# Performance work log

Measured on AMD Instinct MI355X. Metric: run time of the kernel, lower is better.

## Reference

```python
import jax, jax.numpy as jnp
import numpy as np
import math

B, U, IN, H = 4096, 6, 256, 600
IKS, IVS, NIH = 64, 400, 1           # input attention key/value sizes, heads
CKS, CQS, NCH = 32, 32, 4            # comm attention key/query sizes, heads
CVS = H                              # comm value size forced to hidden_size
K = 4                                # top-k active units


@jax.custom_vjp
def blocked_grad(x, mask):
    return x

def _bg_fwd(x, mask):
    return x, mask

def _bg_bwd(mask, g):
    return (g * mask, jnp.zeros_like(mask))

blocked_grad.defvjp(_bg_fwd, _bg_bwd)


def _gll(x, w):
    # GroupLinearLayer: per-unit bmm, x (B,U,din) @ w (U,din,dout) -> (B,U,dout)
    return jnp.einsum('bud,udo->buo', x, w)


def setup_inputs() -> dict:
    key = jax.random.key(0)
    ks = jax.random.split(key, 16)
    r = lambda i, shape: (0.02 * jax.random.normal(ks[i], shape)).astype(jnp.float32)
    return dict(
        x=jax.random.normal(ks[0], (B, 1, IN), jnp.float32),
        hs=jax.random.normal(ks[1], (B, U, H), jnp.float32),
        Wk=r(2, (IN, NIH * IKS)), bk=jnp.zeros((NIH * IKS,), jnp.float32),
        Wv=r(3, (IN, NIH * IVS)), bv=jnp.zeros((NIH * IVS,), jnp.float32),
        Wq=r(4, (U, H, NIH * IKS)),
        x2h_w=r(5, (U, IVS, 3 * H)), h2h_w=r(6, (U, H, 3 * H)),
        Wq_=r(7, (U, H, NCH * CQS)), Wk_=r(8, (U, H, NCH * CKS)),
        Wv_=r(9, (U, H, NCH * CVS)), Wout=r(10, (U, NCH * CVS, CVS)),
    )


def reference(x, hs, Wk, bk, Wv, bv, Wq, x2h_w, h2h_w, Wq_, Wk_, Wv_, Wout):
    h_old = hs
    # append null input along dim 1 -> (B,2,IN)
    xcat = jnp.concatenate([x, jnp.zeros_like(x)], axis=1)
    # ---- input attention + top-k mask ----
    key_l = (xcat @ Wk + bk).reshape(B, 2, NIH, IKS).transpose(0, 2, 1, 3)   # (B,1,2,ks)
    val_l = (xcat @ Wv + bv).reshape(B, 2, NIH, IVS).mean(axis=2)             # (B,2,vs) mean over heads
    qry_l = _gll(hs, Wq).reshape(B, U, NIH, IKS).transpose(0, 2, 1, 3)        # (B,1,U,ks)
    scores = jnp.einsum('bhuk,bhnk->bhun', qry_l, key_l) / math.sqrt(IKS)
    scores = scores.mean(axis=1)                                               # (B,U,2)
    not_null = scores[:, :, 0]
    _, idx = jax.lax.top_k(not_null, K)                                        # (B,K)
    mask = jnp.zeros((B, U), jnp.float32).at[jnp.arange(B)[:, None], idx].set(1.0)
    probs = jax.nn.softmax(scores, axis=-1)                                    # dropout is identity (eval)
    inputs = jnp.einsum('bun,bnv->buv', probs, val_l) * mask[:, :, None]       # (B,U,vs)
    # ---- GroupGRU cell ----
    gx = _gll(inputs, x2h_w)
    gh = _gll(hs, h2h_w)
    i_r, i_i, i_n = jnp.split(gx, 3, axis=2)
    h_r, h_i, h_n = jnp.split(gh, 3, axis=2)
    rg = jax.nn.sigmoid(i_r + h_r)
    ig = jax.nn.sigmoid(i_i + h_i)
    ng = jnp.tanh(i_n + rg * h_n)
    hs = ng + ig * (hs - ng)
    # ---- communication attention (with blocked_grad) ----
    h_b = blocked_grad(hs, mask[:, :, None])
    q = _gll(h_b, Wq_).reshape(B, U, NCH, CQS).transpose(0, 2, 1, 3)   # (B,4,U,32)
    k = _gll(h_b, Wk_).reshape(B, U, NCH, CKS).transpose(0, 2, 1, 3)
    v = _gll(h_b, Wv_).reshape(B, U, NCH, CVS).transpose(0, 2, 1, 3)   # (B,4,U,600)
    att = jax.nn.softmax(jnp.einsum('bhuk,bhnk->bhun', q, k) / math.sqrt(CKS), axis=-1)
    att = att * mask[:, None, :, None]   # zero rows of inactive query units
    ctx = jnp.einsum('bhun,bhnv->bhuv', att, v).transpose(0, 2, 1, 3).reshape(B, U, NCH * CVS)
    ctx = _gll(ctx, Wout) + h_b
    m = mask[:, :, None]
    return m * ctx + (1.0 - m) * h_old
```

## Files before the change

kernel.cpp:

```cpp
#include <hip/hip_runtime.h>
#include <math.h>

typedef unsigned short u16;
typedef __attribute__((ext_vector_type(8))) short short8;
typedef __attribute__((ext_vector_type(4))) float f32x4;

constexpr int NB   = 4096;
constexpr int NU   = 6;
constexpr int NIN  = 256;
constexpr int NH   = 600;
constexpr int IKS  = 64;
constexpr int IVS  = 400;
constexpr int NCH  = 4;
constexpr int CVS  = 600;
constexpr int KTOP = 4;

constexpr int KVW  = IKS + IVS;
constexpr int QKW  = 256;
constexpr int VW   = NCH * CVS;

constexpr int KGRU = 1024;
constexpr int HOFS = 416;
constexpr int NGATE = 640;
constexpr int KH   = 640;
constexpr int VN   = 2432;
constexpr int BC   = 2048;
constexpr int NCHUNK = NB / BC;

constexpr long OFF_KV   = 0;
constexpr long OFF_QRY  = OFF_KV   + (long)NB * KVW;
constexpr long OFF_C0   = OFF_QRY  + (long)NB * NU * IKS;
constexpr long OFF_C1   = OFF_C0   + (long)NB * NU;
constexpr long OFF_MASK = OFF_C1   + (long)NB * NU;
constexpr long OFF_QK   = OFF_MASK + (long)NB * NU;
constexpr long OFF_ATTW = OFF_QK   + (long)NB * NU * QKW;
constexpr long OFF_HNBF = OFF_ATTW + (long)NB * NCH * NU * NU;
constexpr long OFF_WQK  = OFF_HNBF + (long)NU * NB * KH / 2;
constexpr long OFF_WV   = OFF_WQK  + (long)NU * QKW * KH / 2;
constexpr long OFF_WOUT = OFF_WV   + (long)NU * VN * KH / 2;
constexpr long OFF_WGRU = OFF_WOUT + (long)NU * NGATE * VN / 2;
constexpr long OFF_AGRU = OFF_WGRU + (long)NU * 3 * NGATE * KGRU / 2;
constexpr long OFF_VBUF = OFF_WGRU;

__device__ __forceinline__ u16 f2bf(float f) {
    unsigned int x = __float_as_uint(f);
    x += 0x7FFFu + ((x >> 16) & 1u);
    return (u16)(x >> 16);
}
__device__ __forceinline__ float bf2f(u16 u) {
    return __uint_as_float(((unsigned int)u) << 16);
}
__device__ __forceinline__ void gl_lds16(const u16* g, u16* l) {
    __builtin_amdgcn_global_load_lds(
        (const __attribute__((address_space(1))) void*)g,
        (__attribute__((address_space(3))) void*)l, 16, 0, 0);
}
__device__ __forceinline__ void xcd_swz(int& bx, int& by, int& bz)
{
    const int gx = gridDim.x, gy = gridDim.y, gz = gridDim.z;
    const int n = gx * gy * gz;
    if (n & 7) return;
    int lid = bx + gx * (by + gy * bz);
    const int q = n >> 3;
    int w = (lid & 7) * q + (lid >> 3);
    bx = w % gx; int rest = w / gx;
    by = rest % gy; bz = rest / gy;
}

#define WAITVM_(N) asm volatile("s_waitcnt vmcnt(" #N ")" ::: "memory")
#define WAITVM(N)  WAITVM_(N)
#define WAITLG()   asm volatile("s_waitcnt lgkmcnt(0)" ::: "memory")
#define SBAR()     do { __builtin_amdgcn_sched_barrier(0); \
                        __builtin_amdgcn_s_barrier();      \
                        __builtin_amdgcn_sched_barrier(0); } while (0)

__global__ __launch_bounds__(256)
void wtrans_kernel(const float* __restrict__ src, long s_u, int s_ld, int s_colofs,
                   int Ksrc, int Nsub,
                   u16* __restrict__ dst, long d_u, int d_ld, int d_nofs, int d_kofs,
                   int gdiv, int s_gcol, int d_gnofs)
{
    __shared__ float tile[32][33];
    int z = blockIdx.z;
    int u = z, g = 0;
    if (gdiv > 1) { u = z / gdiv; g = z % gdiv; }
    const int k0 = blockIdx.x * 32, n0 = blockIdx.y * 32;
    const int t  = threadIdx.x;
    const int scol = s_colofs + g * s_gcol;
    const int dnof = d_nofs + g * d_gnofs;
    const float* S = src + (long)u * s_u;
    u16* D = dst + (long)u * d_u;
    #pragma unroll
    for (int r = 0; r < 4; r++) {
        int kk = r * 8 + (t >> 5), nn = t & 31;
        float v = 0.f;
        if (k0 + kk < Ksrc && n0 + nn < Nsub)
            v = S[(long)(k0 + kk) * s_ld + scol + n0 + nn];
        tile[kk][nn] = v;
    }
    __syncthreads();
    #pragma unroll
    for (int r = 0; r < 4; r++) {
        int nn = r * 8 + (t >> 5), kk = t & 31;
        if (n0 + nn < Nsub)
            D[(long)(dnof + n0 + nn) * d_ld + d_kofs + k0 + kk] = f2bf(tile[kk][nn]);
    }
}

__global__ __launch_bounds__(256)
void gemm_kv_kernel(const float* __restrict__ x,
                    const float* __restrict__ Wk, const float* __restrict__ bk,
                    const float* __restrict__ Wv, const float* __restrict__ bv,
                    float* __restrict__ kvout)
{
    const int m0 = blockIdx.x * 64;
    const int n0 = blockIdx.y * 64;
    const int tid = threadIdx.x;
    const int tm = tid / 16, tn = tid % 16;
    constexpr int K = NIN, N = KVW;

    __shared__ __align__(16) float As[32][72];
    __shared__ __align__(16) float Ws[32][68];
    float acc[4][4] = {};

    for (int k0 = 0; k0 < K; k0 += 32) {
        #pragma unroll
        for (int s2 = 0; s2 < 2; s2++) {
            int s = tid * 2 + s2;
            int row = s >> 3, kc = s & 7;
            float4 v = *(const float4*)&x[(long)(m0 + row) * K + k0 + kc * 4];
            As[kc*4+0][row] = v.x; As[kc*4+1][row] = v.y;
            As[kc*4+2][row] = v.z; As[kc*4+3][row] = v.w;
        }
        #pragma unroll
        for (int s2 = 0; s2 < 2; s2++) {
            int s = tid * 2 + s2;
            int kr = s >> 4, c4 = s & 15;
            int cg = n0 + c4 * 4;
            float4 v = {0,0,0,0};
            if (cg < IKS)    v = *(const float4*)&Wk[(long)(k0+kr)*IKS + cg];
            else if (cg < N) v = *(const float4*)&Wv[(long)(k0+kr)*IVS + (cg - IKS)];
            *(float4*)&Ws[kr][c4*4] = v;
        }
        __syncthreads();
        #pragma unroll
        for (int kk = 0; kk < 32; kk++) {
            float4 a4 = *(const float4*)&As[kk][tm*4];
            float4 w4 = *(const float4*)&Ws[kk][tn*4];
            float av[4] = {a4.x,a4.y,a4.z,a4.w}, wv[4] = {w4.x,w4.y,w4.z,w4.w};
            #pragma unroll
            for (int i = 0; i < 4; i++)
                #pragma unroll
                for (int j = 0; j < 4; j++)
                    acc[i][j] = fmaf(av[i], wv[j], acc[i][j]);
        }
        __syncthreads();
    }
    #pragma unroll
    for (int i = 0; i < 4; i++) {
        int row = m0 + tm*4 + i;
        #pragma unroll
        for (int j = 0; j < 4; j++) {
            int cg = n0 + tn*4 + j;
            if (cg < N) {
                float bias = (cg < IKS) ? bk[cg] : bv[cg - IKS];
                kvout[(long)row*N + cg] = acc[i][j] + bias;
            }
        }
    }
}

__global__ __launch_bounds__(256)
void gemm_qry_kernel(const float* __restrict__ A,
                     const float* __restrict__ W,
                     float* __restrict__ C)
{
    const int u  = blockIdx.z;
    const int m0 = blockIdx.x * 64;
    const int tid = threadIdx.x;
    const int tm = tid / 16, tn = tid % 16;
    constexpr int K = NH, N = IKS;
    const long lda = (long)NU * NH;

    __shared__ __align__(16) float As[32][72];
    __shared__ __align__(16) float Ws[32][68];
    const float* Au = A + (long)u * K;
    const float* Wu = W + (long)u * K * N;
    float acc[4][4] = {};

    for (int k0 = 0; k0 < K; k0 += 32) {
        #pragma unroll
        for (int s2 = 0; s2 < 2; s2++) {
            int s = tid * 2 + s2;
            int row = s >> 3, kc = s & 7;
            float4 v = {0,0,0,0};
            if (k0 + kc*4 < K)
                v = *(const float4*)&Au[(long)(m0 + row) * lda + k0 + kc * 4];
            As[kc*4+0][row] = v.x; As[kc*4+1][row] = v.y;
            As[kc*4+2][row] = v.z; As[kc*4+3][row] = v.w;
        }
        #pragma unroll
        for (int s2 = 0; s2 < 2; s2++) {
            int s = tid * 2 + s2;
            int kr = s >> 4, c4 = s & 15;
            float4 v = {0,0,0,0};
            if (k0 + kr < K)
                v = *(const float4*)&Wu[(long)(k0 + kr) * N + c4 * 4];
            *(float4*)&Ws[kr][c4*4] = v;
        }
        __syncthreads();
        #pragma unroll
        for (int kk = 0; kk < 32; kk++) {
            float4 a4 = *(const float4*)&As[kk][tm*4];
            float4 w4 = *(const float4*)&Ws[kk][tn*4];
            float av[4] = {a4.x,a4.y,a4.z,a4.w}, wv[4] = {w4.x,w4.y,w4.z,w4.w};
            #pragma unroll
            for (int i = 0; i < 4; i++)
                #pragma unroll
                for (int j = 0; j < 4; j++)
                    acc[i][j] = fmaf(av[i], wv[j], acc[i][j]);
        }
        __syncthreads();
    }
    #pragma unroll
    for (int i = 0; i < 4; i++) {
        int row = m0 + tm*4 + i;
        #pragma unroll
        for (int j = 0; j < 4; j++) {
            int c = tn*4 + j;
            C[(long)row*(NU*IKS) + (long)u*IKS + c] = acc[i][j];
        }
    }
}

__global__ __launch_bounds__(64)
void score_kernel(const float* __restrict__ qry, const float* __restrict__ kv,
                  const float* __restrict__ bk,
                  float* __restrict__ c0, float* __restrict__ c1,
                  float* __restrict__ maskf)
{
    const int b = blockIdx.x;
    const int t = threadIdx.x;
    __shared__ float s0s[NU], s1s[NU];

    float k0v = kv[(long)b*KVW + t];
    float bkv = bk[t];
    for (int u = 0; u < NU; u++) {
        float q  = qry[((long)b*NU + u)*IKS + t];
        float p0 = q * k0v, p1 = q * bkv;
        #pragma unroll
        for (int off = 32; off > 0; off >>= 1) {
            p0 += __shfl_down(p0, off);
            p1 += __shfl_down(p1, off);
        }
        if (t == 0) { s0s[u] = p0 * 0.125f; s1s[u] = p1 * 0.125f; }
    }
    __syncthreads();
    if (t < NU) {
        int u = t;
        float su = s0s[u];
        int rank = 0;
        #pragma unroll
        for (int j = 0; j < NU; j++) {
            float sj = s0s[j];
            if (sj > su || (sj == su && j < u)) rank++;
        }
        float m = (rank < KTOP) ? 1.0f : 0.0f;
        float a = s0s[u], bb = s1s[u];
        float mx = fmaxf(a, bb);
        float e0 = expf(a - mx), e1 = expf(bb - mx);
        float p0 = e0 / (e0 + e1);
        c0[(long)b*NU + u]    = m * p0;
        c1[(long)b*NU + u]    = m * (1.0f - p0);
        maskf[(long)b*NU + u] = m;
    }
}

__global__ __launch_bounds__(256)
void prep_gruA_kernel(const float* __restrict__ kv, const float* __restrict__ bv,
                      const float* __restrict__ hs,
                      const float* __restrict__ c0, const float* __restrict__ c1,
                      u16* __restrict__ Ag)
{
    long id = (long)blockIdx.x * 256 + threadIdx.x;
    const long total = (long)NU * NB * (KGRU / 8);
    if (id >= total) return;
    int k8 = (int)(id % (KGRU / 8));
    int b  = (int)((id / (KGRU / 8)) % NB);
    int u  = (int)(id / ((long)(KGRU / 8) * NB));
    int k  = k8 * 8;
    u16 o[8];
    if (k < IVS) {
        float cv0 = c0[(long)b*NU + u], cv1 = c1[(long)b*NU + u];
        const float* kp = kv + (long)b*KVW + IKS + k;
        const float* bp = bv + k;
        #pragma unroll
        for (int i = 0; i < 8; i++) o[i] = f2bf(cv0*kp[i] + cv1*bp[i]);
    } else if (k >= HOFS && k < HOFS + NH) {
        const float* hp = hs + ((long)b*NU + u)*NH + (k - HOFS);
        #pragma unroll
        for (int i = 0; i < 8; i++) o[i] = f2bf(hp[i]);
    } else {
        #pragma unroll
        for (int i = 0; i < 8; i++) o[i] = 0;
    }
    *(short8*)&Ag[id * 8] = *(const short8*)o;
}

__global__ __launch_bounds__(256, 3)
void gru_mfma_kernel(const u16* __restrict__ Ag, const u16* __restrict__ Wg,
                     const float* __restrict__ hs, u16* __restrict__ hnbf)
{
    int bx = blockIdx.x, by = blockIdx.y, bz = blockIdx.z;
    xcd_swz(bx, by, bz);
    const int u  = bz;
    const int m0 = bx * 128;
    const int n0 = by * 32;
    const int tid = threadIdx.x;
    const int wid = tid >> 6, lane = tid & 63;
    const int wm = wid >> 1, wn = wid & 1;
    const int lrow = lane & 15, lkq = lane >> 4;
    const int srow = lane >> 2;
    const int scs  = (((lane & 3) ^ ((lane >> 3) & 3)) * 8);
    const int cofs = ((lkq ^ ((lrow >> 1) & 3)) * 8);

    __shared__ __align__(16) u16 As[3][128 * 32];
    __shared__ __align__(16) u16 Bs[3][128 * 32];

    const u16* Au = Ag + (long)u * NB * KGRU;
    const u16* Wu = Wg + (long)u * 3 * NGATE * KGRU;

    f32x4 aR[4], aI[4], aNX[4], aNH[4];
    #pragma unroll
    for (int m = 0; m < 4; m++) {
        aR[m] = (f32x4){0,0,0,0}; aI[m] = (f32x4){0,0,0,0};
        aNX[m] = (f32x4){0,0,0,0}; aNH[m] = (f32x4){0,0,0,0};
    }

#define GSTAGE(BUF, T) do {                                                   \
        const long kk0 = (long)(T) * 32;                                      \
        _Pragma("unroll")                                                     \
        for (int i2 = 0; i2 < 2; i2++) {                                      \
            int R = wid*32 + i2*16;                                           \
            int row = R + srow;                                               \
            gl_lds16(Au + (long)(m0 + row)*KGRU + kk0 + scs,                  \
                     &As[BUF][R * 32]);                                       \
            int g = row >> 5; if (g > 2) g = 2;     \
            int rn = row & 31;                                                \
            gl_lds16(Wu + ((long)g*NGATE + n0 + rn)*KGRU + kk0 + scs,         \
                     &Bs[BUF][R * 32]);                                       \
        }                                                                     \
    } while (0)

#define GCOMPUTE(BUF, T) do {                                                 \
        __builtin_amdgcn_s_setprio(1);                                        \
        short8 af[4], bR, bI, bN;                                             \
        _Pragma("unroll")                                                     \
        for (int m = 0; m < 4; m++)                                           \
            af[m] = *(const short8*)&As[BUF][(wm*64 + m*16 + lrow)*32 + cofs];\
        {                                                                     \
            int nr = wn*16 + lrow;                                            \
            bR = *(const short8*)&Bs[BUF][(0*32 + nr)*32 + cofs];             \
            bI = *(const short8*)&Bs[BUF][(1*32 + nr)*32 + cofs];             \
            bN = *(const short8*)&Bs[BUF][(2*32 + nr)*32 + cofs];             \
        }                                                                     \
        _Pragma("unroll")                                                     \
        for (int m = 0; m < 4; m++) {                                         \
            aR[m] = __builtin_amdgcn_mfma_f32_16x16x32_bf16(af[m], bR, aR[m], 0, 0, 0); \
            aI[m] = __builtin_amdgcn_mfma_f32_16x16x32_bf16(af[m], bI, aI[m], 0, 0, 0); \
        }                                                                     \
        if ((T) < HOFS/32) {                                                  \
            _Pragma("unroll")                                                 \
            for (int m = 0; m < 4; m++)                                       \
                aNX[m] = __builtin_amdgcn_mfma_f32_16x16x32_bf16(af[m], bN, aNX[m], 0, 0, 0); \
        } else {                                                              \
            _Pragma("unroll")                                                 \
            for (int m = 0; m < 4; m++)                                       \
                aNH[m] = __builtin_amdgcn_mfma_f32_16x16x32_bf16(af[m], bN, aNH[m], 0, 0, 0); \
        }                                                                     \
        __builtin_amdgcn_s_setprio(0);                                        \
    } while (0)

    constexpr int KSTEPS = KGRU / 32;
    GSTAGE(0, 0);
    int bc = 0, bn = 1;
    for (int t = 0; t < KSTEPS - 1; ++t) {
        GSTAGE(bn, t + 1);
        WAITVM(4); SBAR();
        GCOMPUTE(bc, t);
        bc = bn; bn = (bn == 2) ? 0 : bn + 1;
    }
    WAITVM(0); SBAR();
    GCOMPUTE(bc, KSTEPS - 1);
#undef GCOMPUTE
#undef GSTAGE

    #pragma unroll
    for (int m = 0; m < 4; m++) {
        #pragma unroll
        for (int r = 0; r < 4; r++) {
            int row = m0 + wm*64 + m*16 + lkq*4 + r;
            int col = n0 + wn*16 + lrow;
            u16 ov = 0;
            if (col < NH) {
                float rg = 1.0f / (1.0f + expf(-aR[m][r]));
                float ig = 1.0f / (1.0f + expf(-aI[m][r]));
                float ng = tanhf(aNX[m][r] + rg * aNH[m][r]);
                float h  = hs[((long)row*NU + u)*NH + col];
                ov = f2bf(ng + ig * (h - ng));
            }
            hnbf[(long)u*NB*KH + (long)row*KH + col] = ov;
        }
    }
}

template<int EPI>
__global__ __launch_bounds__(256, 2)
void mfgemm_kernel(const u16* __restrict__ A, long sAu, int lda,
                   const u16* __restrict__ Bw, long sBu, int ldb,
                   float* __restrict__ Cf, u16* __restrict__ C16,
                   long sCu, int ldc, int ksteps,
                   const float* __restrict__ maskf,
                   const u16* __restrict__ hnbf,
                   const float* __restrict__ hs,
                   int bbase)
{
    int bx = blockIdx.x, by = blockIdx.y, bz = blockIdx.z;
    xcd_swz(bx, by, bz);
    const int u  = bz;
    const int m0 = bx * 128;
    const int n0 = by * 128;
    const int tid = threadIdx.x;
    const int wid = tid >> 6, lane = tid & 63;
    const int wm = wid >> 1, wn = wid & 1;
    const int lrow = lane & 15, lkq = lane >> 4;
    const int l8 = lane & 7, lr8 = lane >> 3;
    const int rsw = lrow & 7;

    __shared__ __align__(16) u16 As[2][128 * 64];
    __shared__ __align__(16) u16 Bs[2][128 * 64];

    const u16* Au = A + (long)u * sAu;
    const u16* Bu = Bw + (long)u * sBu;

    f32x4 acc[4][4];
    #pragma unroll
    for (int m = 0; m < 4; m++)
        #pragma unroll
        for (int n = 0; n < 4; n++) acc[m][n] = (f32x4){0,0,0,0};

#define MSTAGE(BUF, KS) do {                                                  \
        const long kk0 = (long)(KS) * 64;                                     \
        _Pragma("unroll")                                                     \
        for (int i2 = 0; i2 < 4; i2++) {                                      \
            int rw = i2*32 + wid*8 + lr8;                                     \
            int co = ((l8 ^ (rw & 7)) * 8);                                   \
            gl_lds16(Au + (long)(m0 + rw)*lda + kk0 + co,                     \
                     &As[BUF][(i2*32 + wid*8) * 64]);                         \
            gl_lds16(Bu + (long)(n0 + rw)*ldb + kk0 + co,                     \
                     &Bs[BUF][(i2*32 + wid*8) * 64]);                         \
        }                                                                     \
    } while (0)

#define MCOMPUTE(BUF) do {                                                    \
        __builtin_amdgcn_s_setprio(1);                                        \
        _Pragma("unroll")                                                     \
        for (int ks2 = 0; ks2 < 2; ks2++) {                                   \
            const int cofs = (((ks2*4 + lkq) ^ rsw) * 8);                     \
            short8 af[4], bfr[4];                                             \
            _Pragma("unroll")                                                 \
            for (int m = 0; m < 4; m++)                                       \
                af[m] = *(const short8*)&As[BUF][(wm*64 + m*16 + lrow)*64 + cofs]; \
            _Pragma("unroll")                                                 \
            for (int n = 0; n < 4; n++)                                       \
                bfr[n] = *(const short8*)&Bs[BUF][(wn*64 + n*16 + lrow)*64 + cofs]; \
            _Pragma("unroll")                                                 \
            for (int m = 0; m < 4; m++)                                       \
                _Pragma("unroll")                                             \
                for (int n = 0; n < 4; n++)                                   \
                    acc[m][n] = __builtin_amdgcn_mfma_f32_16x16x32_bf16(af[m], bfr[n], acc[m][n], 0, 0, 0); \
        }                                                                     \
        __builtin_amdgcn_s_setprio(0);                                        \
    } while (0)

#define MPH(BUF, T, W) do {                                                   \
        if ((T) + 1 < ksteps) MSTAGE((BUF)^1, (T)+1);                         \
        WAITVM(W); SBAR();                                                    \
        MCOMPUTE(BUF);                                                        \
        WAITLG(); SBAR();                                                     \
    } while (0)

    MSTAGE(0, 0);
    int t = 0;
    for (; t + 2 < ksteps; t += 2) { MPH(0, t, 8); MPH(1, t+1, 8); }
    if (t + 2 == ksteps) { MPH(0, t, 8); MPH(1, t+1, 0); }
    else                 { MPH(0, t, 0); }
#undef MPH
#undef MCOMPUTE
#undef MSTAGE

    #pragma unroll
    for (int m = 0; m < 4; m++) {
        #pragma unroll
        for (int r = 0; r < 4; r++) {
            int row = m0 + wm*64 + m*16 + lkq*4 + r;
            #pragma unroll
            for (int n = 0; n < 4; n++) {
                int col = n0 + wn*64 + n*16 + lrow;
                float v = acc[m][n][r];
                if (EPI == 0) {
                    Cf[(long)u*sCu + (long)row*ldc + col] = v;
                } else if (EPI == 2) {
                    C16[(long)u*sCu + (long)row*ldc + col] = f2bf(v);
                } else {
                    if (col < NH) {
                        int b = bbase + row;
                        long o = ((long)b*NU + u)*NH + col;
                        float mk = maskf[(long)b*NU + u];
                        float hv = bf2f(hnbf[(long)u*NB*KH + (long)b*KH + col]);
                        Cf[o] = (mk > 0.5f) ? (v + hv) : hs[o];
                    }
                }
            }
        }
    }
}

__global__ __launch_bounds__(64)
void attw_kernel(const float* __restrict__ qk, const float* __restrict__ maskf,
                 float* __restrict__ attw)
{
    const int bh = blockIdx.x;
    const int b = bh / NCH, h = bh % NCH;
    const int t = threadIdx.x;
    __shared__ float lg[NU][NU];

    if (t < NU * NU) {
        int uq = t / NU, un = t % NU;
        const float* qp = qk + ((long)b*NU + uq)*QKW + h*32;
        const float* kp = qk + ((long)b*NU + un)*QKW + 128 + h*32;
        float s = 0;
        #pragma unroll
        for (int i = 0; i < 32; i++) s = fmaf(qp[i], kp[i], s);
        lg[uq][un] = s * 0.17677669529663687f;
    }
    __syncthreads();
    if (t < NU) {
        int uq = t;
        float mx = -1e30f;
        #pragma unroll
        for (int n = 0; n < NU; n++) mx = fmaxf(mx, lg[uq][n]);
        float e[NU], se = 0;
        #pragma unroll
        for (int n = 0; n < NU; n++) { e[n] = expf(lg[uq][n] - mx); se += e[n]; }
        float m = maskf[(long)b*NU + uq];
        float inv = m / se;
        #pragma unroll
        for (int n = 0; n < NU; n++)
            attw[(((long)b*NCH + h)*NU + uq)*NU + n] = e[n] * inv;
    }
}

__global__ __launch_bounds__(256)
void ctx2_kernel(const float* __restrict__ attw, u16* vc, int bbase)
{
    __shared__ float att_s[32][NCH * NU * NU];
    const int c0 = blockIdx.x * 64;
    const int b0 = blockIdx.y * 32;
    const int tid = threadIdx.x;

    for (int i = tid; i < 32 * 144; i += 256) {
        int bl = i / 144, j = i % 144;
        att_s[bl][j] = attw[(long)(bbase + b0 + bl) * 144 + j];
    }
    __syncthreads();

    const int bl = tid >> 3;
    const int c  = c0 + (tid & 7) * 8;
    const long rowbase = (long)(b0 + bl) * NU;

    if (c >= VW) {
        short8 z = {0,0,0,0,0,0,0,0};
        #pragma unroll
        for (int u = 0; u < NU; u++)
            *(short8*)&vc[(rowbase + u) * VN + c] = z;
        return;
    }
    const int h = c / CVS;
    const float* aw = &att_s[bl][h * 36];

    float vf[NU][8];
    #pragma unroll
    for (int n = 0; n < NU; n++) {
        short8 vv = *(const short8*)&vc[(rowbase + n) * VN + c];
        #pragma unroll
        for (int i = 0; i < 8; i++) vf[n][i] = bf2f((u16)vv[i]);
    }
    #pragma unroll
    for (int u = 0; u < NU; u++) {
        float acc[8] = {};
        #pragma unroll
        for (int n = 0; n < NU; n++) {
            float a = aw[u * 6 + n];
            #pragma unroll
            for (int i = 0; i < 8; i++) acc[i] = fmaf(a, vf[n][i], acc[i]);
        }
        short8 o;
        #pragma unroll
        for (int i = 0; i < 8; i++) o[i] = (short)f2bf(acc[i]);
        *(short8*)&vc[(rowbase + u) * VN + c] = o;
    }
}

extern "C" void kernel_launch(void* const* d_in, const int* in_sizes, int n_in,
                              void* d_out, int out_size, void* d_ws, size_t ws_size,
                              hipStream_t stream)
{
    const float* x    = (const float*)d_in[0];
    const float* hs   = (const float*)d_in[1];
    const float* Wk   = (const float*)d_in[2];
    const float* bk   = (const float*)d_in[3];
    const float* Wv   = (const float*)d_in[4];
    const float* bv   = (const float*)d_in[5];
    const float* Wq   = (const float*)d_in[6];
    const float* x2h  = (const float*)d_in[7];
    const float* h2h  = (const float*)d_in[8];
    const float* Wq_  = (const float*)d_in[9];
    const float* Wk_  = (const float*)d_in[10];
    const float* Wv_  = (const float*)d_in[11];
    const float* Wout = (const float*)d_in[12];
    float* out = (float*)d_out;
    float* ws  = (float*)d_ws;

    float* kv    = ws + OFF_KV;
    float* qry   = ws + OFF_QRY;
    float* c0b   = ws + OFF_C0;
    float* c1b   = ws + OFF_C1;
    float* maskf = ws + OFF_MASK;
    float* qk    = ws + OFF_QK;
    float* attw  = ws + OFF_ATTW;
    u16*   hnbf  = (u16*)(ws + OFF_HNBF);
    u16*   wqk   = (u16*)(ws + OFF_WQK);
    u16*   wv    = (u16*)(ws + OFF_WV);
    u16*   wout  = (u16*)(ws + OFF_WOUT);
    u16*   wgru  = (u16*)(ws + OFF_WGRU);
    u16*   agru  = (u16*)(ws + OFF_AGRU);
    u16*   vcbuf = (u16*)(ws + OFF_VBUF);

    wtrans_kernel<<<dim3(20, 4, NU), 256, 0, stream>>>(
        Wq_, (long)NH*128, 128, 0, NH, 128, wqk, (long)QKW*KH, KH, 0, 0, 1, 0, 0);
    wtrans_kernel<<<dim3(20, 4, NU), 256, 0, stream>>>(
        Wk_, (long)NH*128, 128, 0, NH, 128, wqk, (long)QKW*KH, KH, 128, 0, 1, 0, 0);
    wtrans_kernel<<<dim3(20, 75, NU), 256, 0, stream>>>(
        Wv_, (long)NH*VW, VW, 0, NH, VW, wv, (long)VN*KH, KH, 0, 0, 1, 0, 0);
    wtrans_kernel<<<dim3(76, 19, NU), 256, 0, stream>>>(
        Wout, (long)VW*NH, NH, 0, VW, NH, wout, (long)NGATE*VN, VN, 0, 0, 1, 0, 0);
    wtrans_kernel<<<dim3(13, 19, NU*3), 256, 0, stream>>>(
        x2h, (long)IVS*3*NH, 3*NH, 0, IVS, NH,
        wgru, (long)3*NGATE*KGRU, KGRU, 0, 0, 3, NH, NGATE);
    wtrans_kernel<<<dim3(19, 19, NU*3), 256, 0, stream>>>(
        h2h, (long)NH*3*NH, 3*NH, 0, NH, NH,
        wgru, (long)3*NGATE*KGRU, KGRU, 0, HOFS, 3, NH, NGATE);

    gemm_kv_kernel<<<dim3(NB/64, (KVW+63)/64), 256, 0, stream>>>(x, Wk, bk, Wv, bv, kv);
    gemm_qry_kernel<<<dim3(NB/64, 1, NU), 256, 0, stream>>>(hs, Wq, qry);
    score_kernel<<<NB, 64, 0, stream>>>(qry, kv, bk, c0b, c1b, maskf);

    {
        long total = (long)NU * NB * (KGRU/8);
        prep_gruA_kernel<<<(unsigned)((total + 255)/256), 256, 0, stream>>>(
            kv, bv, hs, c0b, c1b, agru);
    }
    gru_mfma_kernel<<<dim3(NB/128, NGATE/32, NU), 256, 0, stream>>>(agru, wgru, hs, hnbf);

    mfgemm_kernel<0><<<dim3(NB/128, QKW/128, NU), 256, 0, stream>>>(
        hnbf, (long)NB*KH, KH, wqk, (long)QKW*KH, KH,
        qk, nullptr, (long)QKW, NU*QKW, KH/64, nullptr, nullptr, nullptr, 0);
    attw_kernel<<<NB*NCH, 64, 0, stream>>>(qk, maskf, attw);

    for (int ch = 0; ch < NCHUNK; ch++) {
        mfgemm_kernel<2><<<dim3(BC/128, VN/128, NU), 256, 0, stream>>>(
            hnbf + (long)ch*BC*KH, (long)NB*KH, KH, wv, (long)VN*KH, KH,
            nullptr, vcbuf, (long)VN, NU*VN, KH/64, nullptr, nullptr, nullptr, 0);
        ctx2_kernel<<<dim3(VN/64, BC/32), 256, 0, stream>>>(
            attw, vcbuf, ch*BC);
        mfgemm_kernel<1><<<dim3(BC/128, NGATE/128, NU), 256, 0, stream>>>(
            vcbuf, (long)VN, NU*VN, wout, (long)NGATE*VN, VN,
            out, nullptr, 0, 0, VN/64, maskf, hnbf, hs, ch*BC);
    }
}
```

Baseline: 707.8 us.

## Deepen GEMM pipelines to 4-stage ring and drop XCD block swizzle

Both the GRU MFMA kernel and the generic mfgemm kernel now use a 4-buffer LDS ring with two K-steps in flight, waiting on vmcnt(8) instead of the previous shallower schedules. mfgemm moves from K=64 double-buffered tiles to K=32 tiles, taking the GRU kernel's swizzle layout, and drops the trailing lgkmcnt wait and barrier. The XCD block-index swizzle is removed from both kernels, and the GRU kernel's occupancy hint drops from 3 to 2 blocks per CU to fit the larger LDS footprint. The aim is better hiding of global-load latency, at the cost of more barriers per K and possibly worse L2 locality across XCDs.

```diff
diff --git a/kernel.cpp b/kernel.cpp
--- a/kernel.cpp
+++ b/kernel.cpp
@@ -55,21 +55,9 @@
         (const __attribute__((address_space(1))) void*)g,
         (__attribute__((address_space(3))) void*)l, 16, 0, 0);
 }
-__device__ __forceinline__ void xcd_swz(int& bx, int& by, int& bz)
-{
-    const int gx = gridDim.x, gy = gridDim.y, gz = gridDim.z;
-    const int n = gx * gy * gz;
-    if (n & 7) return;
-    int lid = bx + gx * (by + gy * bz);
-    const int q = n >> 3;
-    int w = (lid & 7) * q + (lid >> 3);
-    bx = w % gx; int rest = w / gx;
-    by = rest % gy; bz = rest / gy;
-}
 
 #define WAITVM_(N) asm volatile("s_waitcnt vmcnt(" #N ")" ::: "memory")
 #define WAITVM(N)  WAITVM_(N)
-#define WAITLG()   asm volatile("s_waitcnt lgkmcnt(0)" ::: "memory")
 #define SBAR()     do { __builtin_amdgcn_sched_barrier(0); \
                         __builtin_amdgcn_s_barrier();      \
                         __builtin_amdgcn_sched_barrier(0); } while (0)
@@ -307,15 +295,13 @@
     *(short8*)&Ag[id * 8] = *(const short8*)o;
 }
 
-__global__ __launch_bounds__(256, 3)
+__global__ __launch_bounds__(256, 2)
 void gru_mfma_kernel(const u16* __restrict__ Ag, const u16* __restrict__ Wg,
                      const float* __restrict__ hs, u16* __restrict__ hnbf)
 {
-    int bx = blockIdx.x, by = blockIdx.y, bz = blockIdx.z;
-    xcd_swz(bx, by, bz);
-    const int u  = bz;
-    const int m0 = bx * 128;
-    const int n0 = by * 32;
+    const int u  = blockIdx.z;
+    const int m0 = blockIdx.x * 128;
+    const int n0 = blockIdx.y * 32;
     const int tid = threadIdx.x;
     const int wid = tid >> 6, lane = tid & 63;
     const int wm = wid >> 1, wn = wid & 1;
@@ -324,8 +310,8 @@
     const int scs  = (((lane & 3) ^ ((lane >> 3) & 3)) * 8);
     const int cofs = ((lkq ^ ((lrow >> 1) & 3)) * 8);
 
-    __shared__ __align__(16) u16 As[3][128 * 32];
-    __shared__ __align__(16) u16 Bs[3][128 * 32];
+    __shared__ __align__(16) u16 As[4][128 * 32];
+    __shared__ __align__(16) u16 Bs[4][128 * 32];
 
     const u16* Au = Ag + (long)u * NB * KGRU;
     const u16* Wu = Wg + (long)u * 3 * NGATE * KGRU;
@@ -383,15 +369,16 @@
 
     constexpr int KSTEPS = KGRU / 32;
     GSTAGE(0, 0);
-    int bc = 0, bn = 1;
-    for (int t = 0; t < KSTEPS - 1; ++t) {
-        GSTAGE(bn, t + 1);
-        WAITVM(4); SBAR();
-        GCOMPUTE(bc, t);
-        bc = bn; bn = (bn == 2) ? 0 : bn + 1;
-    }
+    GSTAGE(1, 1);
+    for (int t = 0; t < KSTEPS - 2; ++t) {
+        GSTAGE((t + 2) & 3, t + 2);
+        WAITVM(8); SBAR();
+        GCOMPUTE(t & 3, t);
+    }
+    WAITVM(4); SBAR();
+    GCOMPUTE((KSTEPS - 2) & 3, KSTEPS - 2);
     WAITVM(0); SBAR();
-    GCOMPUTE(bc, KSTEPS - 1);
+    GCOMPUTE((KSTEPS - 1) & 3, KSTEPS - 1);
 #undef GCOMPUTE
 #undef GSTAGE
 
@@ -425,20 +412,19 @@
                    const float* __restrict__ hs,
                    int bbase)
 {
-    int bx = blockIdx.x, by = blockIdx.y, bz = blockIdx.z;
-    xcd_swz(bx, by, bz);
-    const int u  = bz;
-    const int m0 = bx * 128;
-    const int n0 = by * 128;
+    const int u  = blockIdx.z;
+    const int m0 = blockIdx.x * 128;
+    const int n0 = blockIdx.y * 128;
     const int tid = threadIdx.x;
     const int wid = tid >> 6, lane = tid & 63;
     const int wm = wid >> 1, wn = wid & 1;
     const int lrow = lane & 15, lkq = lane >> 4;
-    const int l8 = lane & 7, lr8 = lane >> 3;
-    const int rsw = lrow & 7;
-
-    __shared__ __align__(16) u16 As[2][128 * 64];
-    __shared__ __align__(16) u16 Bs[2][128 * 64];
+    const int srow = lane >> 2;
+    const int scs  = (((lane & 3) ^ ((lane >> 3) & 3)) * 8);
+    const int cofs = ((lkq ^ ((lrow >> 1) & 3)) * 8);
+
+    __shared__ __align__(16) u16 As[4][128 * 32];
+    __shared__ __align__(16) u16 Bs[4][128 * 32];
 
     const u16* Au = A + (long)u * sAu;
     const u16* Bu = Bw + (long)u * sBu;
@@ -449,53 +435,48 @@
         #pragma unroll
         for (int n = 0; n < 4; n++) acc[m][n] = (f32x4){0,0,0,0};
 
-#define MSTAGE(BUF, KS) do {                                                  \
-        const long kk0 = (long)(KS) * 64;                                     \
+#define MSTAGE(BUF, T) do {                                                   \
+        const long kk0 = (long)(T) * 32;                                      \
         _Pragma("unroll")                                                     \
-        for (int i2 = 0; i2 < 4; i2++) {                                      \
-            int rw = i2*32 + wid*8 + lr8;                                     \
-            int co = ((l8 ^ (rw & 7)) * 8);                                   \
-            gl_lds16(Au + (long)(m0 + rw)*lda + kk0 + co,                     \
-                     &As[BUF][(i2*32 + wid*8) * 64]);                         \
-            gl_lds16(Bu + (long)(n0 + rw)*ldb + kk0 + co,                     \
-                     &Bs[BUF][(i2*32 + wid*8) * 64]);                         \
+        for (int i2 = 0; i2 < 2; i2++) {                                      \
+            int R = wid*32 + i2*16;                                           \
+            int row = R + srow;                                               \
+            gl_lds16(Au + (long)(m0 + row)*lda + kk0 + scs,                   \
+                     &As[BUF][R * 32]);                                       \
+            gl_lds16(Bu + (long)(n0 + row)*ldb + kk0 + scs,                   \
+                     &Bs[BUF][R * 32]);                                       \
         }                                                                     \
     } while (0)
 
 #define MCOMPUTE(BUF) do {                                                    \
         __builtin_amdgcn_s_setprio(1);                                        \
+        short8 af[4], bfr[4];                                                 \
         _Pragma("unroll")                                                     \
-        for (int ks2 = 0; ks2 < 2; ks2++) {                                   \
-            const int cofs = (((ks2*4 + lkq) ^ rsw) * 8);                     \
-            short8 af[4], bfr[4];                                             \
-            _Pragma("unroll")                                                 \
-            for (int m = 0; m < 4; m++)                                       \
-                af[m] = *(const short8*)&As[BUF][(wm*64 + m*16 + lrow)*64 + cofs]; \
+        for (int m = 0; m < 4; m++)                                           \
+            af[m] = *(const short8*)&As[BUF][(wm*64 + m*16 + lrow)*32 + cofs];\
+        _Pragma("unroll")                                                     \
+        for (int n = 0; n < 4; n++)                                           \
+            bfr[n] = *(const short8*)&Bs[BUF][(wn*64 + n*16 + lrow)*32 + cofs];\
+        _Pragma("unroll")                                                     \
+        for (int m = 0; m < 4; m++)                                           \
             _Pragma("unroll")                                                 \
             for (int n = 0; n < 4; n++)                                       \
-                bfr[n] = *(const short8*)&Bs[BUF][(wn*64 + n*16 + lrow)*64 + cofs]; \
-            _Pragma("unroll")                                                 \
-            for (int m = 0; m < 4; m++)                                       \
-                _Pragma("unroll")                                             \
-                for (int n = 0; n < 4; n++)                                   \
-                    acc[m][n] = __builtin_amdgcn_mfma_f32_16x16x32_bf16(af[m], bfr[n], acc[m][n], 0, 0, 0); \
-        }                                                                     \
+                acc[m][n] = __builtin_amdgcn_mfma_f32_16x16x32_bf16(af[m], bfr[n], acc[m][n], 0, 0, 0); \
         __builtin_amdgcn_s_setprio(0);                                        \
     } while (0)
 
-#define MPH(BUF, T, W) do {                                                   \
-        if ((T) + 1 < ksteps) MSTAGE((BUF)^1, (T)+1);                         \
-        WAITVM(W); SBAR();                                                    \
-        MCOMPUTE(BUF);                                                        \
-        WAITLG(); SBAR();                                                     \
-    } while (0)
-
     MSTAGE(0, 0);
+    MSTAGE(1, 1);
     int t = 0;
-    for (; t + 2 < ksteps; t += 2) { MPH(0, t, 8); MPH(1, t+1, 8); }
-    if (t + 2 == ksteps) { MPH(0, t, 8); MPH(1, t+1, 0); }
-    else                 { MPH(0, t, 0); }
-#undef MPH
+    for (; t < ksteps - 2; ++t) {
+        MSTAGE((t + 2) & 3, t + 2);
+        WAITVM(8); SBAR();
+        MCOMPUTE(t & 3);
+    }
+    WAITVM(4); SBAR();
+    MCOMPUTE(t & 3); ++t;
+    WAITVM(0); SBAR();
+    MCOMPUTE(t & 3);
 #undef MCOMPUTE
 #undef MSTAGE
 
@@ -675,17 +656,17 @@
 
     mfgemm_kernel<0><<<dim3(NB/128, QKW/128, NU), 256, 0, stream>>>(
         hnbf, (long)NB*KH, KH, wqk, (long)QKW*KH, KH,
-        qk, nullptr, (long)QKW, NU*QKW, KH/64, nullptr, nullptr, nullptr, 0);
+        qk, nullptr, (long)QKW, NU*QKW, KH/32, nullptr, nullptr, nullptr, 0);
     attw_kernel<<<NB*NCH, 64, 0, stream>>>(qk, maskf, attw);
 
     for (int ch = 0; ch < NCHUNK; ch++) {
         mfgemm_kernel<2><<<dim3(BC/128, VN/128, NU), 256, 0, stream>>>(
             hnbf + (long)ch*BC*KH, (long)NB*KH, KH, wv, (long)VN*KH, KH,
-            nullptr, vcbuf, (long)VN, NU*VN, KH/64, nullptr, nullptr, nullptr, 0);
+            nullptr, vcbuf, (long)VN, NU*VN, KH/32, nullptr, nullptr, nullptr, 0);
         ctx2_kernel<<<dim3(VN/64, BC/32), 256, 0, stream>>>(
             attw, vcbuf, ch*BC);
         mfgemm_kernel<1><<<dim3(BC/128, NGATE/128, NU), 256, 0, stream>>>(
             vcbuf, (long)VN, NU*VN, wout, (long)NGATE*VN, VN,
-            out, nullptr, 0, 0, VN/64, maskf, hnbf, hs, ch*BC);
-    }
-}
+            out, nullptr, 0, 0, VN/32, maskf, hnbf, hs, ch*BC);
+    }
+}
```

Result: slower. 768.8 us (+8.6%).
